# Kernel optimization log

Hardware: AMD Instinct MI355X
Metric: run time of the kernel (lower is better)

The kernel has to match this reference:

```python
import jax, jax.numpy as jnp
import numpy as np

B, S, D = 4, 2048, 1024
H = 16
HD = D // H  # head_dim = key_dim = value_dim = 64


def setup_inputs() -> dict:
    key = jax.random.key(0)
    ks = jax.random.split(key, 4)
    scale = (2.0 / (D + D)) ** 0.5  # xavier_normal for square weight
    return {
        "hidden_states": jax.random.normal(ks[0], (B, S, D), dtype=jnp.float32),
        "Wq": jax.random.normal(ks[1], (D, D), dtype=jnp.float32) * scale,
        "bq": jnp.zeros((D,), dtype=jnp.float32),
        "Wk": jax.random.normal(ks[2], (D, D), dtype=jnp.float32) * scale,
        "bk": jnp.zeros((D,), dtype=jnp.float32),
        "Wv": jax.random.normal(ks[3], (D, D), dtype=jnp.float32) * scale,
        "bv": jnp.zeros((D,), dtype=jnp.float32),
    }


def _split_heads(x):
    # [B, S, H*HD] -> [B, H, S, HD]
    b, s, _ = x.shape
    return x.reshape(b, s, H, HD).transpose(0, 2, 1, 3)


def reference(hidden_states, Wq, bq, Wk, bk, Wv, bv):
    # Linear projections (torch Linear: x @ W.T + b)
    q = _split_heads(hidden_states @ Wq.T + bq)  # [B,H,S,HD]
    k = _split_heads(hidden_states @ Wk.T + bk)
    v = _split_heads(hidden_states @ Wv.T + bv)
    scores = jnp.einsum("bhqd,bhkd->bhqk", q, k) / jnp.sqrt(jnp.float32(HD))
    probs = jax.nn.softmax(scores, axis=-1)
    out = jnp.einsum("bhqk,bhkd->bhqd", probs, v)  # [B,H,S,HD]
    # merge heads -> [B, S, H*HD]
    return out.transpose(0, 2, 1, 3).reshape(B, S, H * HD)
```

## Files before the change

kernel.cpp:

```cpp
#include <hip/hip_runtime.h>
#include <math.h>

#define SB 4
#define SS 2048
#define SD 1024
#define SH 16
#define SHD 64
#define SM (SB * SS)

using f32x4 = __attribute__((ext_vector_type(4))) float;
using h8    = __attribute__((ext_vector_type(8))) _Float16;
using h4    = __attribute__((ext_vector_type(4))) _Float16;
using fp16x2 = __fp16 __attribute__((ext_vector_type(2)));
using fp16x4 = __fp16 __attribute__((ext_vector_type(4)));

__device__ __forceinline__ unsigned short f2h(float x) {
  _Float16 h = (_Float16)x;
  return __builtin_bit_cast(unsigned short, h);
}

__device__ __forceinline__ void gld_lds16(const unsigned short* g, unsigned short* l) {
  __builtin_amdgcn_global_load_lds(
      (const __attribute__((address_space(1))) unsigned int*)g,
      (__attribute__((address_space(3))) unsigned int*)l, 16, 0, 0);
}

__global__ __launch_bounds__(256) void cvt4h(const float* __restrict__ in,
                                             unsigned short* __restrict__ out, int n4) {
  int i = blockIdx.x * 256 + threadIdx.x;
  if (i >= n4) return;
  float4 v = ((const float4*)in)[i];
  unsigned long long r = (unsigned long long)f2h(v.x)
                       | ((unsigned long long)f2h(v.y) << 16)
                       | ((unsigned long long)f2h(v.z) << 32)
                       | ((unsigned long long)f2h(v.w) << 48);
  ((unsigned long long*)out)[i] = r;
}

__global__ __launch_bounds__(256) void cvt3w(const float* __restrict__ w0, const float* __restrict__ w1,
                                             const float* __restrict__ w2,
                                             unsigned short* __restrict__ o0, unsigned short* __restrict__ o1,
                                             unsigned short* __restrict__ o2) {
  const int z = blockIdx.y;
  const float* in = (z == 0) ? w0 : (z == 1) ? w1 : w2;
  unsigned short* out = (z == 0) ? o0 : (z == 1) ? o1 : o2;
  int i = blockIdx.x * 256 + threadIdx.x;
  float4 v = ((const float4*)in)[i];
  unsigned long long r = (unsigned long long)f2h(v.x)
                       | ((unsigned long long)f2h(v.y) << 16)
                       | ((unsigned long long)f2h(v.z) << 32)
                       | ((unsigned long long)f2h(v.w) << 48);
  ((unsigned long long*)out)[i] = r;
}

__global__ __launch_bounds__(256) void gemm_qkv(
    const unsigned short* __restrict__ Xh,
    const unsigned short* __restrict__ Wqh, const unsigned short* __restrict__ Wkh,
    const unsigned short* __restrict__ Wvh,
    const float* __restrict__ bq, const float* __restrict__ bk, const float* __restrict__ bv,
    unsigned short* __restrict__ Qh, unsigned short* __restrict__ Kh,
    unsigned short* __restrict__ Vt) {
  __shared__ unsigned short lA[128 * 64];
  __shared__ unsigned short lB[128 * 64];
  const int L = blockIdx.x;
  const int xcd = L & 7, rr = L >> 3;
  const int mloc = rr & 7, widx = rr >> 3;
  const int tNi = widx & 7, z = widx >> 3;
  const int tM = (xcd * 8 + mloc) * 128, tN = tNi * 128;

  const unsigned short* W = (z == 0) ? Wqh : (z == 1) ? Wkh : Wvh;
  const float* bias = (z == 0) ? bq : (z == 1) ? bk : bv;

  const int tid = threadIdx.x;
  const int wave = tid >> 6, lane = tid & 63;
  const int quad = lane >> 4, l16 = lane & 15;
  const int wr = (wave >> 1) * 64, wc = (wave & 1) * 64;

  f32x4 acc[4][4] = {};

  const int rB = tid >> 3;
  const int colOff = (((tid & 7) ^ (rB & 7))) * 8;
  const unsigned short* gA[4];
  const unsigned short* gB[4];
#pragma unroll
  for (int i = 0; i < 4; ++i) {
    gA[i] = Xh + (size_t)(tM + i * 32 + rB) * SD + colOff;
    gB[i] = W  + (size_t)(tN + i * 32 + rB) * SD + colOff;
  }
  unsigned short* dA[4];
  unsigned short* dB[4];
#pragma unroll
  for (int i = 0; i < 4; ++i) {
    dA[i] = lA + (i * 256 + wave * 64) * 8;
    dB[i] = lB + (i * 256 + wave * 64) * 8;
  }
  const int swl = l16 & 7;

  for (int k0 = 0; k0 < SD; k0 += 64) {
    __syncthreads();
#pragma unroll
    for (int i = 0; i < 4; ++i) gld_lds16(gA[i] + k0, dA[i]);
#pragma unroll
    for (int i = 0; i < 4; ++i) gld_lds16(gB[i] + k0, dB[i]);
    __syncthreads();

#pragma unroll
    for (int ks = 0; ks < 2; ++ks) {
      h8 af[4], bf[4];
#pragma unroll
      for (int mi = 0; mi < 4; ++mi)
        af[mi] = *(const h8*)(lA + (wr + mi * 16 + l16) * 64 + (((ks * 4 + quad) ^ swl) * 8));
#pragma unroll
      for (int ni = 0; ni < 4; ++ni)
        bf[ni] = *(const h8*)(lB + (wc + ni * 16 + l16) * 64 + (((ks * 4 + quad) ^ swl) * 8));
#pragma unroll
      for (int mi = 0; mi < 4; ++mi)
#pragma unroll
        for (int ni = 0; ni < 4; ++ni)
          acc[mi][ni] = __builtin_amdgcn_mfma_f32_16x16x32_f16(af[mi], bf[ni], acc[mi][ni], 0, 0, 0);
    }
  }

  if (z == 2) {
#pragma unroll
    for (int ni = 0; ni < 4; ++ni) {
      const int gn = tN + wc + ni * 16 + l16;
      const float bb = bias[gn];
#pragma unroll
      for (int mi = 0; mi < 4; ++mi) {
        const int gm = tM + wr + mi * 16 + quad * 4;
        const int vb = gm >> 11, vs = gm & 2047;
        unsigned long long wv = 0;
#pragma unroll
        for (int r = 0; r < 4; ++r)
          wv |= (unsigned long long)f2h(acc[mi][ni][r] + bb) << (16 * r);
        *(unsigned long long*)(Vt + (size_t)(vb * 1024 + gn) * SS + vs) = wv;
      }
    }
  } else {
    const float sc = (z == 0) ? 0.18033688011112042f : 1.0f;
    unsigned short* C = (z == 0) ? Qh : Kh;
#pragma unroll
    for (int ni = 0; ni < 4; ++ni) {
      const int gn = tN + wc + ni * 16 + l16;
      const float bb = bias[gn];
#pragma unroll
      for (int mi = 0; mi < 4; ++mi)
#pragma unroll
        for (int r = 0; r < 4; ++r) {
          const int gm = tM + wr + mi * 16 + quad * 4 + r;
          C[(size_t)gm * SD + gn] = f2h((acc[mi][ni][r] + bb) * sc);
        }
    }
  }
}

__global__ __launch_bounds__(256, 4) void attn(const unsigned short* __restrict__ Qh,
                                               const unsigned short* __restrict__ Kh,
                                               const unsigned short* __restrict__ Vt,
                                               float* __restrict__ out) {
  __shared__ unsigned short lK[2][64 * 64];
  __shared__ unsigned short lV[2][64 * 64];
  const int tid = threadIdx.x;
  const int wave = tid >> 6, lane = tid & 63;
  const int quad = lane >> 4, l16 = lane & 15;
  const int qh = quad >> 1, ql = quad & 1;
  const int bid = blockIdx.x;
  const int bh = (bid & 7) | (((bid >> 3) & 7) << 3);
  const int qt = bid >> 6;
  const int b = bh >> 4, h = bh & 15;
  const int qsA = qt * 128 + wave * 16;

  const unsigned short* qpA = Qh + ((size_t)(b * SS + qsA + l16)) * SD + h * 64 + quad * 8;
  const unsigned short* qpB = qpA + (size_t)64 * SD;
  h8 aqA0 = *(const h8*)(qpA);
  h8 aqA1 = *(const h8*)(qpA + 32);
  h8 aqB0 = *(const h8*)(qpB);
  h8 aqB1 = *(const h8*)(qpB + 32);

  const int row0 = tid >> 3, cs0 = (tid & 7) ^ (row0 & 7);
  const int row1 = row0 + 32, cs1 = (tid & 7) ^ (row1 & 7);
  const unsigned short* kS0 = Kh + ((size_t)(b * SS + row0)) * SD + h * 64 + cs0 * 8;
  const unsigned short* kS1 = Kh + ((size_t)(b * SS + row1)) * SD + h * 64 + cs1 * 8;
  const unsigned short* vS0 = Vt + ((size_t)(bh * 64 + row0)) * SS + cs0 * 8;
  const unsigned short* vS1 = Vt + ((size_t)(bh * 64 + row1)) * SS + cs1 * 8;
  unsigned short* dK0 = &lK[0][wave * 512];
  unsigned short* dK1 = &lK[0][2048 + wave * 512];
  unsigned short* dV0 = &lV[0][wave * 512];
  unsigned short* dV1 = &lV[0][2048 + wave * 512];

  f32x4 ovA[4] = {}, ovB[4] = {};
  float l_accA = 0.f, l_accB = 0.f;
  const int swl = l16 & 7;

  gld_lds16(kS0, dK0); gld_lds16(kS1, dK1);
  gld_lds16(vS0, dV0); gld_lds16(vS1, dV1);
  kS0 += 64 * SD; kS1 += 64 * SD; vS0 += 64; vS1 += 64;

  for (int kt = 0; kt < 32; ++kt) {
    const int buf = kt & 1;
    __syncthreads();
    if (kt < 31) {
      const int o = (buf ^ 1) * 64 * 64;
      gld_lds16(kS0, dK0 + o); gld_lds16(kS1, dK1 + o);
      gld_lds16(vS0, dV0 + o); gld_lds16(vS1, dV1 + o);
      kS0 += 64 * SD; kS1 += 64 * SD; vS0 += 64; vS1 += 64;
    }
    const unsigned short* Kt = lK[buf];
    const unsigned short* Vl = lV[buf];

    f32x4 sA[4], sB[4];
#pragma unroll
    for (int nt = 0; nt < 4; ++nt) {
      const unsigned short* kr = Kt + (nt * 16 + l16) * 64;
      h8 kf0 = *(const h8*)(kr + ((quad ^ swl) * 8));
      h8 kf1 = *(const h8*)(kr + (((4 + quad) ^ swl) * 8));
      f32x4 zA = {};
      zA = __builtin_amdgcn_mfma_f32_16x16x32_f16(kf0, aqA0, zA, 0, 0, 0);
      sA[nt] = __builtin_amdgcn_mfma_f32_16x16x32_f16(kf1, aqA1, zA, 0, 0, 0);
      f32x4 zB = {};
      zB = __builtin_amdgcn_mfma_f32_16x16x32_f16(kf0, aqB0, zB, 0, 0, 0);
      sB[nt] = __builtin_amdgcn_mfma_f32_16x16x32_f16(kf1, aqB1, zB, 0, 0, 0);
    }

#pragma unroll
    for (int g = 0; g < 4; ++g) {
      h4 vf[4];
#pragma unroll
      for (int f = 0; f < 4; ++f) {
        h8 vv = *(const h8*)(Vl + (f * 16 + l16) * 64 + (((g * 2 + qh) ^ swl) * 8));
        h4 lo = __builtin_shufflevector(vv, vv, 0, 1, 2, 3);
        h4 hi = __builtin_shufflevector(vv, vv, 4, 5, 6, 7);
        vf[f] = ql ? hi : lo;
      }
      {
        float p0 = __builtin_amdgcn_exp2f(sA[g][0]);
        float p1 = __builtin_amdgcn_exp2f(sA[g][1]);
        float p2 = __builtin_amdgcn_exp2f(sA[g][2]);
        float p3 = __builtin_amdgcn_exp2f(sA[g][3]);
        l_accA += (p0 + p1) + (p2 + p3);
        fp16x2 lo = __builtin_amdgcn_cvt_pkrtz(p0, p1);
        fp16x2 hi = __builtin_amdgcn_cvt_pkrtz(p2, p3);
        h4 pp = __builtin_bit_cast(h4, __builtin_shufflevector(lo, hi, 0, 1, 2, 3));
#pragma unroll
        for (int f = 0; f < 4; ++f)
          ovA[f] = __builtin_amdgcn_mfma_f32_16x16x16f16(vf[f], pp, ovA[f], 0, 0, 0);
      }
      {
        float p0 = __builtin_amdgcn_exp2f(sB[g][0]);
        float p1 = __builtin_amdgcn_exp2f(sB[g][1]);
        float p2 = __builtin_amdgcn_exp2f(sB[g][2]);
        float p3 = __builtin_amdgcn_exp2f(sB[g][3]);
        l_accB += (p0 + p1) + (p2 + p3);
        fp16x2 lo = __builtin_amdgcn_cvt_pkrtz(p0, p1);
        fp16x2 hi = __builtin_amdgcn_cvt_pkrtz(p2, p3);
        h4 pp = __builtin_bit_cast(h4, __builtin_shufflevector(lo, hi, 0, 1, 2, 3));
#pragma unroll
        for (int f = 0; f < 4; ++f)
          ovB[f] = __builtin_amdgcn_mfma_f32_16x16x16f16(vf[f], pp, ovB[f], 0, 0, 0);
      }
    }
  }
  float ltA = l_accA;
  ltA += __shfl_xor(ltA, 16);
  ltA += __shfl_xor(ltA, 32);
  const float invA = 1.0f / ltA;
  float ltB = l_accB;
  ltB += __shfl_xor(ltB, 16);
  ltB += __shfl_xor(ltB, 32);
  const float invB = 1.0f / ltB;
  float* orowA = out + ((size_t)(b * SS + qsA + l16)) * SD + h * 64 + quad * 4;
  float* orowB = orowA + (size_t)64 * SD;
#pragma unroll
  for (int f = 0; f < 4; ++f) {
    float4 w;
    w.x = ovA[f][0] * invA; w.y = ovA[f][1] * invA;
    w.z = ovA[f][2] * invA; w.w = ovA[f][3] * invA;
    *(float4*)(orowA + f * 16) = w;
    float4 u;
    u.x = ovB[f][0] * invB; u.y = ovB[f][1] * invB;
    u.z = ovB[f][2] * invB; u.w = ovB[f][3] * invB;
    *(float4*)(orowB + f * 16) = u;
  }
}

extern "C" void kernel_launch(void* const* d_in, const int* in_sizes, int n_in,
                              void* d_out, int out_size, void* d_ws, size_t ws_size,
                              hipStream_t stream) {
  const float* hs = (const float*)d_in[0];
  const float* Wq = (const float*)d_in[1];
  const float* bq = (const float*)d_in[2];
  const float* Wk = (const float*)d_in[3];
  const float* bk = (const float*)d_in[4];
  const float* Wv = (const float*)d_in[5];
  const float* bv = (const float*)d_in[6];
  float* out = (float*)d_out;

  char* ws = (char*)d_ws;
  unsigned short* Xh  = (unsigned short*)(ws);
  unsigned short* Wqh = (unsigned short*)(ws + 16777216);
  unsigned short* Wkh = (unsigned short*)(ws + 16777216 + 2097152);
  unsigned short* Wvh = (unsigned short*)(ws + 16777216 + 2 * 2097152);
  unsigned short* Qh  = (unsigned short*)(ws + 16777216 + 3 * 2097152);
  unsigned short* Kh  = Qh + (size_t)SM * SD;
  unsigned short* Vt  = Kh + (size_t)SM * SD;

  cvt4h<<<dim3(8192), dim3(256), 0, stream>>>(hs, Xh, SM * SD / 4);
  cvt3w<<<dim3(1024, 3), dim3(256), 0, stream>>>(Wq, Wk, Wv, Wqh, Wkh, Wvh);
  gemm_qkv<<<dim3(1536), dim3(256), 0, stream>>>(
      Xh, Wqh, Wkh, Wvh, bq, bk, bv, Qh, Kh, Vt);
  attn<<<dim3(SB * SH * (SS / 128)), dim3(256), 0, stream>>>(Qh, Kh, Vt, out);
}
```

Baseline: 257.5 us.

## Stage P through LDS for 16x16x32 PV MFMA and vectorize Q/K stores

In attention, the probability tiles are written to a per-wave LDS scratch buffer and re-read in the layout the 16x16x32 MFMA expects. This replaces the 16x16x16 PV MFMAs and the per-element V half-selection with half as many K=32 MFMAs. The Q/K projection swaps the MFMA operand order so each lane holds contiguous columns, allowing packed 64-bit stores and a float4 bias load instead of scalar 16-bit stores. The cost is extra LDS traffic and lgkmcnt waits for the P round-trip, plus duplicated GEMM loop code.

```diff
diff --git a/kernel.cpp b/kernel.cpp
--- a/kernel.cpp
+++ b/kernel.cpp
@@ -96,32 +96,30 @@
   }
   const int swl = l16 & 7;
 
-  for (int k0 = 0; k0 < SD; k0 += 64) {
-    __syncthreads();
-#pragma unroll
-    for (int i = 0; i < 4; ++i) gld_lds16(gA[i] + k0, dA[i]);
-#pragma unroll
-    for (int i = 0; i < 4; ++i) gld_lds16(gB[i] + k0, dB[i]);
-    __syncthreads();
-
-#pragma unroll
-    for (int ks = 0; ks < 2; ++ks) {
-      h8 af[4], bf[4];
-#pragma unroll
-      for (int mi = 0; mi < 4; ++mi)
-        af[mi] = *(const h8*)(lA + (wr + mi * 16 + l16) * 64 + (((ks * 4 + quad) ^ swl) * 8));
-#pragma unroll
-      for (int ni = 0; ni < 4; ++ni)
-        bf[ni] = *(const h8*)(lB + (wc + ni * 16 + l16) * 64 + (((ks * 4 + quad) ^ swl) * 8));
-#pragma unroll
-      for (int mi = 0; mi < 4; ++mi)
+  if (z == 2) {
+    for (int k0 = 0; k0 < SD; k0 += 64) {
+      __syncthreads();
+#pragma unroll
+      for (int i = 0; i < 4; ++i) gld_lds16(gA[i] + k0, dA[i]);
+#pragma unroll
+      for (int i = 0; i < 4; ++i) gld_lds16(gB[i] + k0, dB[i]);
+      __syncthreads();
+#pragma unroll
+      for (int ks = 0; ks < 2; ++ks) {
+        h8 af[4], bf[4];
+#pragma unroll
+        for (int mi = 0; mi < 4; ++mi)
+          af[mi] = *(const h8*)(lA + (wr + mi * 16 + l16) * 64 + (((ks * 4 + quad) ^ swl) * 8));
 #pragma unroll
         for (int ni = 0; ni < 4; ++ni)
-          acc[mi][ni] = __builtin_amdgcn_mfma_f32_16x16x32_f16(af[mi], bf[ni], acc[mi][ni], 0, 0, 0);
-    }
-  }
-
-  if (z == 2) {
+          bf[ni] = *(const h8*)(lB + (wc + ni * 16 + l16) * 64 + (((ks * 4 + quad) ^ swl) * 8));
+#pragma unroll
+        for (int mi = 0; mi < 4; ++mi)
+#pragma unroll
+          for (int ni = 0; ni < 4; ++ni)
+            acc[mi][ni] = __builtin_amdgcn_mfma_f32_16x16x32_f16(af[mi], bf[ni], acc[mi][ni], 0, 0, 0);
+      }
+    }
 #pragma unroll
     for (int ni = 0; ni < 4; ++ni) {
       const int gn = tN + wc + ni * 16 + l16;
@@ -138,19 +136,45 @@
       }
     }
   } else {
+    for (int k0 = 0; k0 < SD; k0 += 64) {
+      __syncthreads();
+#pragma unroll
+      for (int i = 0; i < 4; ++i) gld_lds16(gA[i] + k0, dA[i]);
+#pragma unroll
+      for (int i = 0; i < 4; ++i) gld_lds16(gB[i] + k0, dB[i]);
+      __syncthreads();
+#pragma unroll
+      for (int ks = 0; ks < 2; ++ks) {
+        h8 af[4], bf[4];
+#pragma unroll
+        for (int mi = 0; mi < 4; ++mi)
+          af[mi] = *(const h8*)(lA + (wr + mi * 16 + l16) * 64 + (((ks * 4 + quad) ^ swl) * 8));
+#pragma unroll
+        for (int ni = 0; ni < 4; ++ni)
+          bf[ni] = *(const h8*)(lB + (wc + ni * 16 + l16) * 64 + (((ks * 4 + quad) ^ swl) * 8));
+#pragma unroll
+        for (int mi = 0; mi < 4; ++mi)
+#pragma unroll
+          for (int ni = 0; ni < 4; ++ni)
+            acc[mi][ni] = __builtin_amdgcn_mfma_f32_16x16x32_f16(bf[ni], af[mi], acc[mi][ni], 0, 0, 0);
+      }
+    }
     const float sc = (z == 0) ? 0.18033688011112042f : 1.0f;
     unsigned short* C = (z == 0) ? Qh : Kh;
 #pragma unroll
-    for (int ni = 0; ni < 4; ++ni) {
-      const int gn = tN + wc + ni * 16 + l16;
-      const float bb = bias[gn];
-#pragma unroll
-      for (int mi = 0; mi < 4; ++mi)
-#pragma unroll
-        for (int r = 0; r < 4; ++r) {
-          const int gm = tM + wr + mi * 16 + quad * 4 + r;
-          C[(size_t)gm * SD + gn] = f2h((acc[mi][ni][r] + bb) * sc);
-        }
+    for (int mi = 0; mi < 4; ++mi) {
+      const int gm = tM + wr + mi * 16 + l16;
+#pragma unroll
+      for (int ni = 0; ni < 4; ++ni) {
+        const int gnb = tN + wc + ni * 16 + quad * 4;
+        const float4 bb4 = *(const float4*)(bias + gnb);
+        unsigned long long wv;
+        wv  = (unsigned long long)f2h((acc[mi][ni][0] + bb4.x) * sc);
+        wv |= (unsigned long long)f2h((acc[mi][ni][1] + bb4.y) * sc) << 16;
+        wv |= (unsigned long long)f2h((acc[mi][ni][2] + bb4.z) * sc) << 32;
+        wv |= (unsigned long long)f2h((acc[mi][ni][3] + bb4.w) * sc) << 48;
+        *(unsigned long long*)(C + (size_t)gm * SD + gnb) = wv;
+      }
     }
   }
 }
@@ -161,6 +185,7 @@
                                                float* __restrict__ out) {
   __shared__ unsigned short lK[2][64 * 64];
   __shared__ unsigned short lV[2][64 * 64];
+  __shared__ unsigned short pl[4 * 16 * 64];
   const int tid = threadIdx.x;
   const int wave = tid >> 6, lane = tid & 63;
   const int quad = lane >> 4, l16 = lane & 15;
@@ -192,6 +217,9 @@
   f32x4 ovA[4] = {}, ovB[4] = {};
   float l_accA = 0.f, l_accB = 0.f;
   const int swl = l16 & 7;
+  unsigned short* plw = pl + wave * 1024;
+  unsigned short* pwr = plw + l16 * 64;
+  unsigned short* pwrW = pwr + ql * 4;
 
   gld_lds16(kS0, dK0); gld_lds16(kS1, dK1);
   gld_lds16(vS0, dV0); gld_lds16(vS1, dV1);
@@ -225,40 +253,47 @@
 
 #pragma unroll
     for (int g = 0; g < 4; ++g) {
-      h4 vf[4];
-#pragma unroll
-      for (int f = 0; f < 4; ++f) {
-        h8 vv = *(const h8*)(Vl + (f * 16 + l16) * 64 + (((g * 2 + qh) ^ swl) * 8));
-        h4 lo = __builtin_shufflevector(vv, vv, 0, 1, 2, 3);
-        h4 hi = __builtin_shufflevector(vv, vv, 4, 5, 6, 7);
-        vf[f] = ql ? hi : lo;
-      }
-      {
-        float p0 = __builtin_amdgcn_exp2f(sA[g][0]);
-        float p1 = __builtin_amdgcn_exp2f(sA[g][1]);
-        float p2 = __builtin_amdgcn_exp2f(sA[g][2]);
-        float p3 = __builtin_amdgcn_exp2f(sA[g][3]);
-        l_accA += (p0 + p1) + (p2 + p3);
-        fp16x2 lo = __builtin_amdgcn_cvt_pkrtz(p0, p1);
-        fp16x2 hi = __builtin_amdgcn_cvt_pkrtz(p2, p3);
-        h4 pp = __builtin_bit_cast(h4, __builtin_shufflevector(lo, hi, 0, 1, 2, 3));
-#pragma unroll
-        for (int f = 0; f < 4; ++f)
-          ovA[f] = __builtin_amdgcn_mfma_f32_16x16x16f16(vf[f], pp, ovA[f], 0, 0, 0);
-      }
-      {
-        float p0 = __builtin_amdgcn_exp2f(sB[g][0]);
-        float p1 = __builtin_amdgcn_exp2f(sB[g][1]);
-        float p2 = __builtin_amdgcn_exp2f(sB[g][2]);
-        float p3 = __builtin_amdgcn_exp2f(sB[g][3]);
-        l_accB += (p0 + p1) + (p2 + p3);
-        fp16x2 lo = __builtin_amdgcn_cvt_pkrtz(p0, p1);
-        fp16x2 hi = __builtin_amdgcn_cvt_pkrtz(p2, p3);
-        h4 pp = __builtin_bit_cast(h4, __builtin_shufflevector(lo, hi, 0, 1, 2, 3));
-#pragma unroll
-        for (int f = 0; f < 4; ++f)
-          ovB[f] = __builtin_amdgcn_mfma_f32_16x16x16f16(vf[f], pp, ovB[f], 0, 0, 0);
-      }
+      float p0 = __builtin_amdgcn_exp2f(sA[g][0]);
+      float p1 = __builtin_amdgcn_exp2f(sA[g][1]);
+      float p2 = __builtin_amdgcn_exp2f(sA[g][2]);
+      float p3 = __builtin_amdgcn_exp2f(sA[g][3]);
+      l_accA += (p0 + p1) + (p2 + p3);
+      fp16x2 lo = __builtin_amdgcn_cvt_pkrtz(p0, p1);
+      fp16x2 hi = __builtin_amdgcn_cvt_pkrtz(p2, p3);
+      fp16x4 pk = __builtin_shufflevector(lo, hi, 0, 1, 2, 3);
+      *(unsigned long long*)(pwrW + ((2 * g + qh) ^ swl) * 8) =
+          __builtin_bit_cast(unsigned long long, pk);
+    }
+    asm volatile("s_waitcnt lgkmcnt(0)" ::: "memory");
+    h8 pbA0 = *(const h8*)(pwr + ((quad ^ swl) * 8));
+    h8 pbA1 = *(const h8*)(pwr + (((4 + quad) ^ swl) * 8));
+
+#pragma unroll
+    for (int g = 0; g < 4; ++g) {
+      float p0 = __builtin_amdgcn_exp2f(sB[g][0]);
+      float p1 = __builtin_amdgcn_exp2f(sB[g][1]);
+      float p2 = __builtin_amdgcn_exp2f(sB[g][2]);
+      float p3 = __builtin_amdgcn_exp2f(sB[g][3]);
+      l_accB += (p0 + p1) + (p2 + p3);
+      fp16x2 lo = __builtin_amdgcn_cvt_pkrtz(p0, p1);
+      fp16x2 hi = __builtin_amdgcn_cvt_pkrtz(p2, p3);
+      fp16x4 pk = __builtin_shufflevector(lo, hi, 0, 1, 2, 3);
+      *(unsigned long long*)(pwrW + ((2 * g + qh) ^ swl) * 8) =
+          __builtin_bit_cast(unsigned long long, pk);
+    }
+    asm volatile("s_waitcnt lgkmcnt(0)" ::: "memory");
+    h8 pbB0 = *(const h8*)(pwr + ((quad ^ swl) * 8));
+    h8 pbB1 = *(const h8*)(pwr + (((4 + quad) ^ swl) * 8));
+
+#pragma unroll
+    for (int f = 0; f < 4; ++f) {
+      const unsigned short* vr = Vl + (f * 16 + l16) * 64;
+      h8 v0 = *(const h8*)(vr + ((quad ^ swl) * 8));
+      h8 v1 = *(const h8*)(vr + (((4 + quad) ^ swl) * 8));
+      ovA[f] = __builtin_amdgcn_mfma_f32_16x16x32_f16(v0, pbA0, ovA[f], 0, 0, 0);
+      ovA[f] = __builtin_amdgcn_mfma_f32_16x16x32_f16(v1, pbA1, ovA[f], 0, 0, 0);
+      ovB[f] = __builtin_amdgcn_mfma_f32_16x16x32_f16(v0, pbB0, ovB[f], 0, 0, 0);
+      ovB[f] = __builtin_amdgcn_mfma_f32_16x16x32_f16(v1, pbB1, ovB[f], 0, 0, 0);
     }
   }
   float ltA = l_accA;
```

Measured after the change: 251.1 us. 1.03x faster.
